# Kernel tuning notes

Measured on AMD Instinct MI355X. Metric: run time of the kernel, lower is better.

The kernel has to match this reference:

```python
import jax, jax.numpy as jnp
import numpy as np

B, T, DIM, DIM_EPS, H = 4, 1024, 2048, 2048, 16
HD = DIM // H        # 128, value head dim
HDE = DIM_EPS // H   # 128, q/k head dim


def setup_inputs() -> dict:
    key = jax.random.key(0)
    ks = jax.random.split(key, 6)
    s = 0.02
    # rotary frequencies as in llama-style precompute (theta=10000)
    inv_freq = 1.0 / (10000.0 ** (np.arange(0, HDE, 2, dtype=np.float32) / HDE))
    t = np.arange(T, dtype=np.float32)
    ang = np.outer(t, inv_freq)  # (T, HDE//2)
    return {
        "v": jax.random.normal(ks[0], (B, T, DIM), jnp.float32),
        "x_eps": jax.random.normal(ks[1], (B, T, DIM_EPS), jnp.float32),
        "freqs_cos": jnp.asarray(np.cos(ang)),
        "freqs_sin": jnp.asarray(np.sin(ang)),
        "W_eps_attn": jax.random.normal(ks[2], (DIM_EPS, 2 * DIM_EPS), jnp.float32) * s,
        "W_attn": jax.random.normal(ks[3], (DIM, DIM), jnp.float32) * s,
        "W_proj": jax.random.normal(ks[4], (DIM, DIM), jnp.float32) * s,
        "W_eps_proj": jax.random.normal(ks[5], (DIM_EPS, DIM_EPS), jnp.float32) * s,
    }


def _rope(x, cos, sin):
    # x: (B, T, H, HDE) -> complex-multiply by freqs_cis of shape (T, HDE//2)
    xr = x.reshape(*x.shape[:-1], -1, 2)
    x_re, x_im = xr[..., 0], xr[..., 1]
    c = cos[None, :, None, :]  # (1, T, 1, HDE//2)
    s = sin[None, :, None, :]
    o_re = x_re * c - x_im * s
    o_im = x_re * s + x_im * c
    return jnp.stack([o_re, o_im], axis=-1).reshape(x.shape)


def reference(v, x_eps, freqs_cos, freqs_sin, W_eps_attn, W_attn, W_proj, W_eps_proj):
    Bn, Tn, C = v.shape
    qk = x_eps @ W_eps_attn            # (B, T, 2*DIM_EPS)
    q, k = jnp.split(qk, 2, axis=-1)
    vp = v @ W_attn                    # (B, T, DIM)
    q = _rope(q.reshape(Bn, Tn, H, HDE), freqs_cos, freqs_sin)
    k = _rope(k.reshape(Bn, Tn, H, HDE), freqs_cos, freqs_sin)
    q = q.transpose(0, 2, 1, 3)        # (B, H, T, HDE)
    k = k.transpose(0, 2, 1, 3)
    vh = vp.reshape(Bn, Tn, H, HD).transpose(0, 2, 1, 3)
    scale = 1.0 / jnp.sqrt(jnp.asarray(HDE, q.dtype))
    scores = jnp.einsum("bhqd,bhkd->bhqk", q, k) * scale
    causal = jnp.tril(jnp.ones((Tn, Tn), bool))
    scores = jnp.where(causal[None, None], scores, jnp.finfo(scores.dtype).min)
    att = jax.nn.softmax(scores, axis=-1)
    y = jnp.einsum("bhqk,bhkd->bhqd", att, vh)
    y = y.transpose(0, 2, 1, 3).reshape(Bn, Tn, C)
    v_out = y @ W_proj
    x_eps_out = x_eps @ W_eps_proj
    return (v_out, x_eps_out)
```

## Files before the change

### kernel.cpp

```cpp
#include <hip/hip_runtime.h>
#include <stdint.h>

typedef __attribute__((ext_vector_type(8))) short  short8;
typedef __attribute__((ext_vector_type(4))) float  f32x4;
typedef __attribute__((ext_vector_type(4))) float  float4v;
typedef __attribute__((ext_vector_type(4))) unsigned short ushort4v;

#define DEV __device__ __forceinline__

DEV unsigned short f2bf(float f) {
    union { float f; unsigned int u; } x; x.f = f;
    unsigned int u = x.u;
    unsigned int r = (u + 0x7fffu + ((u >> 16) & 1u)) >> 16;
    return (unsigned short)r;
}
DEV float bf2f(unsigned short b) {
    union { unsigned int u; float f; } x; x.u = ((unsigned int)b) << 16;
    return x.f;
}

DEV void gll16(const void* g, void* l) {
    __builtin_amdgcn_global_load_lds(
        (const __attribute__((address_space(1))) void*)g,
        (__attribute__((address_space(3))) void*)l, 16, 0, 0);
}

#define MROWS 4096
#define KDIM  2048
#define NQK   4096

__global__ void cast_f32_bf16(const float* __restrict__ in,
                              unsigned short* __restrict__ out, int n4) {
    int i = blockIdx.x * blockDim.x + threadIdx.x;
    if (i < n4) {
        float4v f = ((const float4v*)in)[i];
        ushort4v o;
        o[0] = f2bf(f[0]); o[1] = f2bf(f[1]); o[2] = f2bf(f[2]); o[3] = f2bf(f[3]);
        ((ushort4v*)out)[i] = o;
    }
}

__global__ void transpose_cast(const float* __restrict__ W,
                               unsigned short* __restrict__ Wt, int K, int N) {
    __shared__ float tile[32][33];
    int tx = threadIdx.x, ty = threadIdx.y;
    int n0 = blockIdx.x * 32, k0 = blockIdx.y * 32;
#pragma unroll
    for (int j = 0; j < 32; j += 8)
        tile[ty + j][tx] = W[(size_t)(k0 + ty + j) * N + n0 + tx];
    __syncthreads();
#pragma unroll
    for (int j = 0; j < 32; j += 8)
        Wt[(size_t)(n0 + ty + j) * K + k0 + tx] = f2bf(tile[tx][ty + j]);
}

__global__ void transpose_v(const unsigned short* __restrict__ vp,
                            unsigned short* __restrict__ vpT) {
    __shared__ unsigned short tile[32][34];
    int tx = threadIdx.x, ty = threadIdx.y;
    int R0 = blockIdx.y * 32;
    int c0 = blockIdx.x * 32;
    int bh = R0 >> 7, d0 = R0 & 127;
    int b = bh >> 4, h = bh & 15;
#pragma unroll
    for (int j = 0; j < 32; j += 8)
        tile[ty + j][tx] = vp[(size_t)(b * 1024 + c0 + ty + j) * 2048 + h * 128 + d0 + tx];
    __syncthreads();
#pragma unroll
    for (int j = 0; j < 32; j += 8)
        vpT[(size_t)(R0 + ty + j) * 1024 + c0 + tx] = tile[tx][ty + j];
}

__global__ __launch_bounds__(512, 2) void gemm256(
    const unsigned short* __restrict__ A0g, const unsigned short* __restrict__ B0g,
    float* __restrict__ Cf0, unsigned short* __restrict__ Ch0,
    int N0, int tx0, int nb0, int outbf0,
    const unsigned short* __restrict__ A1g, const unsigned short* __restrict__ B1g,
    float* __restrict__ Cf1, unsigned short* __restrict__ Ch1,
    int N1, int tx1, int outbf1, int K) {

    __shared__ __align__(16) char lds[131072];

    int blk = blockIdx.x;
    const unsigned short* Ag; const unsigned short* Bg;
    float* Cf; unsigned short* Ch; int N, tx, outbf, nwg;
    if (blk < nb0) { Ag = A0g; Bg = B0g; Cf = Cf0; Ch = Ch0; N = N0; tx = tx0; outbf = outbf0; nwg = nb0; }
    else { blk -= nb0; Ag = A1g; Bg = B1g; Cf = Cf1; Ch = Ch1; N = N1; tx = tx1; outbf = outbf1; nwg = gridDim.x - nb0; }
    { int cpx = nwg >> 3; blk = (blk & 7) * cpx + (blk >> 3); }
    const int bx = blk % tx, by = blk / tx;

    const int tid = threadIdx.x;
    const int lane = tid & 63;
    const int w  = tid >> 6;
    const int lr = lane & 15, lk = lane >> 4;
    const int wm = w >> 2, wn = w & 3;
    const int cswz16 = (lk ^ ((lr >> 3) << 1)) * 16;

    const unsigned short* Arow = Ag + (size_t)(by * 256) * K;
    const unsigned short* Brow = Bg + (size_t)(bx * 256) * K;

    auto STAGE = [&](const unsigned short* srcHalf, int k0, char* ldsHalf) {
        int row  = tid >> 2;
        int clog = (tid & 3) ^ (((tid >> 5) & 1) << 1);
        const unsigned short* g = srcHalf + (size_t)row * K + k0 + clog * 8;
        gll16(g,      ldsHalf + tid * 16);
        gll16(g + 32, ldsHalf + 8192 + tid * 16);
    };

    f32x4 acc[8][4];
#pragma unroll
    for (int m = 0; m < 8; ++m)
#pragma unroll
        for (int n = 0; n < 4; ++n) acc[m][n] = (f32x4){0.f, 0.f, 0.f, 0.f};

    const int NT = K >> 6;
    char* buf0 = lds;
    char* buf1 = lds + 65536;

    STAGE(Brow,                   0, buf0 + 32768);
    STAGE(Brow + (size_t)128 * K, 0, buf0 + 32768 + 16384);
    STAGE(Arow,                   0, buf0);
    STAGE(Arow + (size_t)128 * K, 0, buf0 + 16384);
    STAGE(Brow,                  64, buf1 + 32768);
    STAGE(Brow + (size_t)128 * K, 64, buf1 + 32768 + 16384);
    asm volatile("s_waitcnt vmcnt(4)" ::: "memory");
    __builtin_amdgcn_s_barrier();

#define MFMA_BF(a, b, c) __builtin_amdgcn_mfma_f32_16x16x32_bf16(a, b, c, 0, 0, 0)

#define LDAFR(DST, P)                                                                \
    DST[0] = *(const short8*)(aBase +        ((P) * 32 +      lr) * 64 + cswz16);    \
    DST[1] = *(const short8*)(aBase + 8192 + ((P) * 32 +      lr) * 64 + cswz16);    \
    DST[2] = *(const short8*)(aBase +        ((P) * 32 + 16 + lr) * 64 + cswz16);    \
    DST[3] = *(const short8*)(aBase + 8192 + ((P) * 32 + 16 + lr) * 64 + cswz16);

#define MFMA16(P, R)                                                       \
    __builtin_amdgcn_s_setprio(1);                                         \
    _Pragma("unroll")                                                      \
    for (int nf = 0; nf < 4; ++nf) {                                       \
        acc[2*(P)][nf]   = MFMA_BF(R[0], BC[nf][0], acc[2*(P)][nf]);       \
        acc[2*(P)+1][nf] = MFMA_BF(R[2], BC[nf][0], acc[2*(P)+1][nf]);     \
    }                                                                      \
    _Pragma("unroll")                                                      \
    for (int nf = 0; nf < 4; ++nf) {                                       \
        acc[2*(P)][nf]   = MFMA_BF(R[1], BC[nf][1], acc[2*(P)][nf]);       \
        acc[2*(P)+1][nf] = MFMA_BF(R[3], BC[nf][1], acc[2*(P)+1][nf]);     \
    }                                                                      \
    __builtin_amdgcn_s_setprio(0);

    for (int u = 0; u < NT; ++u) {
        char* bufC = (u & 1) ? buf1 : buf0;
        char* bufN = (u & 1) ? buf0 : buf1;
        const char* aBase = bufC + wm * 16384;
        const char* bBase = bufC + 32768 + (wn >> 1) * 16384;
        const int bRow0 = (wn & 1) * 64;
        const bool stA = (u + 1 < NT), stB = (u + 2 < NT);

        short8 BC[4][2];
#pragma unroll
        for (int nf = 0; nf < 4; ++nf) {
            BC[nf][0] = *(const short8*)(bBase +        (bRow0 + nf * 16 + lr) * 64 + cswz16);
            BC[nf][1] = *(const short8*)(bBase + 8192 + (bRow0 + nf * 16 + lr) * 64 + cswz16);
        }
        short8 Ra[4], Rb[4];
        LDAFR(Ra, 0)
        LDAFR(Rb, 1)
        if (stA) STAGE(Arow, (u + 1) * 64, bufN);
        asm volatile("s_waitcnt lgkmcnt(4)" ::: "memory");
        __builtin_amdgcn_s_barrier();
        MFMA16(0, Ra)
        __builtin_amdgcn_s_barrier();

        LDAFR(Ra, 2)
        if (stA) STAGE(Arow + (size_t)128 * K, (u + 1) * 64, bufN + 16384);
        asm volatile("s_waitcnt lgkmcnt(4)" ::: "memory");
        __builtin_amdgcn_s_barrier();
        MFMA16(1, Rb)
        __builtin_amdgcn_s_barrier();

        LDAFR(Rb, 3)
        if (stB) STAGE(Brow, (u + 2) * 64, bufC + 32768);
        asm volatile("s_waitcnt lgkmcnt(4)" ::: "memory");
        __builtin_amdgcn_s_barrier();
        MFMA16(2, Ra)
        __builtin_amdgcn_s_barrier();

        if (stB) STAGE(Brow + (size_t)128 * K, (u + 2) * 64, bufC + 32768 + 16384);
        asm volatile("s_waitcnt lgkmcnt(0)" ::: "memory");
        __builtin_amdgcn_s_barrier();
        MFMA16(3, Rb)
        if (stB) { asm volatile("s_waitcnt vmcnt(4)" ::: "memory"); }
        else     { asm volatile("s_waitcnt vmcnt(0)" ::: "memory"); }
        __builtin_amdgcn_s_barrier();
    }
#undef LDAFR
#undef MFMA16

    if (outbf) {
#pragma unroll
        for (int mf = 0; mf < 8; ++mf)
#pragma unroll
            for (int nf = 0; nf < 4; ++nf)
#pragma unroll
                for (int r = 0; r < 4; ++r) {
                    int row = by * 256 + wm * 128 + mf * 16 + lk * 4 + r;
                    int col = bx * 256 + wn * 64 + nf * 16 + lr;
                    Ch[(size_t)row * N + col] = f2bf(acc[mf][nf][r]);
                }
    } else {
#pragma unroll
        for (int mf = 0; mf < 8; ++mf)
#pragma unroll
            for (int nf = 0; nf < 4; ++nf)
#pragma unroll
                for (int r = 0; r < 4; ++r) {
                    int row = by * 256 + wm * 128 + mf * 16 + lk * 4 + r;
                    int col = bx * 256 + wn * 64 + nf * 16 + lr;
                    Cf[(size_t)row * N + col] = acc[mf][nf][r];
                }
    }
}

__global__ void rope_kernel(unsigned short* __restrict__ qk,
                            const float* __restrict__ fcos,
                            const float* __restrict__ fsin) {
    int idx  = blockIdx.x * 256 + threadIdx.x;
    int row  = idx >> 9;
    int g    = idx & 511;
    int t    = row & 1023;
    int half = g >> 8;
    int hp   = g & 255;
    int h    = hp >> 4;
    int ig   = hp & 15;
    int col  = half * 2048 + h * 128 + ig * 8;
    size_t off = (size_t)row * 4096 + col;

    short8 v = *(short8*)(qk + off);
    int i0 = ig * 4;
    float4v c = *(const float4v*)(fcos + t * 64 + i0);
    float4v s = *(const float4v*)(fsin + t * 64 + i0);
    short8 o;
#pragma unroll
    for (int p = 0; p < 4; ++p) {
        float re = bf2f((unsigned short)v[2 * p]);
        float im = bf2f((unsigned short)v[2 * p + 1]);
        o[2 * p]     = (short)f2bf(re * c[p] - im * s[p]);
        o[2 * p + 1] = (short)f2bf(re * s[p] + im * c[p]);
    }
    *(short8*)(qk + off) = o;
}

__global__ __launch_bounds__(256) void attn_kernel(
    const unsigned short* __restrict__ qk,
    const unsigned short* __restrict__ vpT,
    unsigned short* __restrict__ y) {

    const int bh = blockIdx.x;
    const int qt = 7 - (int)blockIdx.y;
    const int b = bh >> 4, h = bh & 15;
    const int qb0 = qt * 128;

    __shared__ __align__(16) unsigned short Kt[64 * 128];
    __shared__ __align__(16) unsigned short Vt[128 * 64];
    __shared__ __align__(16) unsigned short Pl[4 * 32 * 72];

    const int tid = threadIdx.x, w = tid >> 6, lane = tid & 63;
    const int lr = lane & 15, lk = lane >> 4;

    const unsigned short* Qb = qk + (size_t)(b * 1024) * 4096 + h * 128;
    const unsigned short* Kb = Qb + 2048;
    const unsigned short* Vg = vpT + (size_t)bh * 128 * 1024;
    unsigned short* Pw = &Pl[w * 32 * 72];

    short8 qf[2][4];
#pragma unroll
    for (int m = 0; m < 2; ++m) {
        const unsigned short* qrow = Qb + (size_t)(qb0 + w * 32 + m * 16 + lr) * 4096;
#pragma unroll
        for (int db = 0; db < 4; ++db)
            qf[m][db] = *(const short8*)(qrow + db * 32 + lk * 8);
    }

    f32x4 acc[2][8];
#pragma unroll
    for (int m = 0; m < 2; ++m)
#pragma unroll
        for (int n = 0; n < 8; ++n) acc[m][n] = (f32x4){0.f, 0.f, 0.f, 0.f};
    float m_i[2][4], l_i[2][4];
#pragma unroll
    for (int m = 0; m < 2; ++m)
#pragma unroll
        for (int r = 0; r < 4; ++r) { m_i[m][r] = -1e30f; l_i[m][r] = 0.f; }

    const int nkt = 2 * qt + 2;
    for (int kt = 0; kt < nkt; ++kt) {
#pragma unroll
        for (int c = 0; c < 4; ++c) {
            int base = w * 4096 + c * 1024;
            int row  = (base >> 8) + (lane >> 4);
            int colB = (lane & 15) * 16;
            int scol = colB ^ ((row & 7) << 4);
            gll16(Kb + (size_t)(kt * 64 + row) * 4096 + (scol >> 1),
                  (char*)Kt + base);
        }
#pragma unroll
        for (int c = 0; c < 4; ++c) {
            int base = w * 4096 + c * 1024;
            int d    = (base >> 7) + (lane >> 3);
            int colB = (lane & 7) * 16;
            int scol = colB ^ ((d & 7) << 4);
            gll16(Vg + (size_t)d * 1024 + kt * 64 + (scol >> 1),
                  (char*)Vt + base);
        }
        __syncthreads();

        f32x4 s[2][4];
#pragma unroll
        for (int m = 0; m < 2; ++m)
#pragma unroll
            for (int n = 0; n < 4; ++n) s[m][n] = (f32x4){0.f, 0.f, 0.f, 0.f};
#pragma unroll
        for (int db = 0; db < 4; ++db)
#pragma unroll
            for (int n = 0; n < 4; ++n) {
                int krow = n * 16 + lr;
                int cb = (db * 64 + lk * 16) ^ ((krow & 7) << 4);
                short8 kf = *(const short8*)((const char*)Kt + krow * 256 + cb);
                s[0][n] = __builtin_amdgcn_mfma_f32_16x16x32_bf16(qf[0][db], kf, s[0][n], 0, 0, 0);
                s[1][n] = __builtin_amdgcn_mfma_f32_16x16x32_bf16(qf[1][db], kf, s[1][n], 0, 0, 0);
            }

        const float sc = 0.08838834764831845f;
        const bool diag = (kt >= 2 * qt);
#pragma unroll
        for (int m = 0; m < 2; ++m)
#pragma unroll
            for (int n = 0; n < 4; ++n)
#pragma unroll
                for (int r = 0; r < 4; ++r) {
                    float v = s[m][n][r] * sc;
                    if (diag) {
                        int q   = qb0 + w * 32 + m * 16 + lk * 4 + r;
                        int key = kt * 64 + n * 16 + lr;
                        if (key > q) v = -1e30f;
                    }
                    s[m][n][r] = v;
                }

#pragma unroll
        for (int m = 0; m < 2; ++m) {
            float pm[4];
#pragma unroll
            for (int r = 0; r < 4; ++r)
                pm[r] = fmaxf(fmaxf(s[m][0][r], s[m][1][r]), fmaxf(s[m][2][r], s[m][3][r]));
#pragma unroll
            for (int o = 1; o < 16; o <<= 1)
#pragma unroll
                for (int r = 0; r < 4; ++r)
                    pm[r] = fmaxf(pm[r], __shfl_xor(pm[r], o, 16));

            float resc[4], rs[4];
#pragma unroll
            for (int r = 0; r < 4; ++r) {
                float mn = fmaxf(m_i[m][r], pm[r]);
                resc[r] = __expf(m_i[m][r] - mn);
                m_i[m][r] = mn;
                rs[r] = 0.f;
            }
#pragma unroll
            for (int n = 0; n < 4; ++n)
#pragma unroll
                for (int r = 0; r < 4; ++r) {
                    float p = __expf(s[m][n][r] - m_i[m][r]);
                    s[m][n][r] = p;
                    rs[r] += p;
                }
#pragma unroll
            for (int o = 1; o < 16; o <<= 1)
#pragma unroll
                for (int r = 0; r < 4; ++r)
                    rs[r] += __shfl_xor(rs[r], o, 16);
#pragma unroll
            for (int r = 0; r < 4; ++r)
                l_i[m][r] = l_i[m][r] * resc[r] + rs[r];
#pragma unroll
            for (int n = 0; n < 8; ++n)
#pragma unroll
                for (int r = 0; r < 4; ++r)
                    acc[m][n][r] *= resc[r];

#pragma unroll
            for (int n = 0; n < 4; ++n)
#pragma unroll
                for (int r = 0; r < 4; ++r)
                    Pw[(m * 16 + lk * 4 + r) * 72 + n * 16 + lr] = f2bf(s[m][n][r]);
        }

#pragma unroll
        for (int ks = 0; ks < 2; ++ks) {
            short8 pf0 = *(const short8*)&Pw[(lr) * 72 + ks * 32 + lk * 8];
            short8 pf1 = *(const short8*)&Pw[(16 + lr) * 72 + ks * 32 + lk * 8];
#pragma unroll
            for (int n8 = 0; n8 < 8; ++n8) {
                int d  = n8 * 16 + lr;
                int cb = (ks * 64 + lk * 16) ^ ((d & 7) << 4);
                short8 vf = *(const short8*)((const char*)Vt + d * 128 + cb);
                acc[0][n8] = __builtin_amdgcn_mfma_f32_16x16x32_bf16(pf0, vf, acc[0][n8], 0, 0, 0);
                acc[1][n8] = __builtin_amdgcn_mfma_f32_16x16x32_bf16(pf1, vf, acc[1][n8], 0, 0, 0);
            }
        }
        __syncthreads();
    }

    unsigned short* yb = y + (size_t)(b * 1024) * 2048 + h * 128;
#pragma unroll
    for (int m = 0; m < 2; ++m)
#pragma unroll
        for (int n8 = 0; n8 < 8; ++n8)
#pragma unroll
            for (int r = 0; r < 4; ++r) {
                int t = qb0 + w * 32 + m * 16 + lk * 4 + r;
                int d = n8 * 16 + lr;
                yb[(size_t)t * 2048 + d] = f2bf(acc[m][n8][r] / l_i[m][r]);
            }
}

extern "C" void kernel_launch(void* const* d_in, const int* in_sizes, int n_in,
                              void* d_out, int out_size, void* d_ws, size_t ws_size,
                              hipStream_t stream) {
    const float* v_in  = (const float*)d_in[0];
    const float* xeps  = (const float*)d_in[1];
    const float* fcos  = (const float*)d_in[2];
    const float* fsin  = (const float*)d_in[3];
    const float* Wea   = (const float*)d_in[4];
    const float* Wa    = (const float*)d_in[5];
    const float* Wp    = (const float*)d_in[6];
    const float* Wep   = (const float*)d_in[7];
    float* out = (float*)d_out;

    char* ws = (char*)d_ws;
    unsigned short* xe16 = (unsigned short*)ws;  ws += (size_t)MROWS * KDIM * 2;
    unsigned short* v16  = (unsigned short*)ws;  ws += (size_t)MROWS * KDIM * 2;
    unsigned short* WeaT = (unsigned short*)ws;  ws += (size_t)NQK * KDIM * 2;
    unsigned short* WaT  = (unsigned short*)ws;  ws += (size_t)KDIM * KDIM * 2;
    unsigned short* WpT  = (unsigned short*)ws;  ws += (size_t)KDIM * KDIM * 2;
    unsigned short* WepT = (unsigned short*)ws;  ws += (size_t)KDIM * KDIM * 2;
    unsigned short* qk16 = (unsigned short*)ws;  ws += (size_t)MROWS * NQK * 2;
    unsigned short* vp16 = (unsigned short*)ws;  ws += (size_t)MROWS * KDIM * 2;
    unsigned short* y16  = (unsigned short*)ws;  ws += (size_t)MROWS * KDIM * 2;
    unsigned short* vpT  = v16;

    cast_f32_bf16<<<8192, 256, 0, stream>>>(xeps, xe16, MROWS * KDIM / 4);
    cast_f32_bf16<<<8192, 256, 0, stream>>>(v_in, v16,  MROWS * KDIM / 4);

    transpose_cast<<<dim3(NQK / 32, KDIM / 32), dim3(32, 8), 0, stream>>>(Wea, WeaT, KDIM, NQK);
    transpose_cast<<<dim3(KDIM / 32, KDIM / 32), dim3(32, 8), 0, stream>>>(Wa,  WaT,  KDIM, KDIM);
    transpose_cast<<<dim3(KDIM / 32, KDIM / 32), dim3(32, 8), 0, stream>>>(Wp,  WpT,  KDIM, KDIM);
    transpose_cast<<<dim3(KDIM / 32, KDIM / 32), dim3(32, 8), 0, stream>>>(Wep, WepT, KDIM, KDIM);

    gemm256<<<256, 512, 0, stream>>>(
        xe16, WeaT, nullptr, qk16, NQK, 16, 256, 1,
        xe16, WeaT, nullptr, qk16, NQK, 16, 1, KDIM);

    rope_kernel<<<8192, 256, 0, stream>>>(qk16, fcos, fsin);

    gemm256<<<256, 512, 0, stream>>>(
        v16,  WaT,  nullptr, vp16, KDIM, 8, 128, 1,
        xe16, WepT, out + (size_t)MROWS * KDIM, nullptr, KDIM, 8, 0, KDIM);

    transpose_v<<<dim3(1024 / 32, 8192 / 32), dim3(32, 8), 0, stream>>>(vp16, vpT);

    attn_kernel<<<dim3(64, 8), 256, 0, stream>>>(qk16, vpT, y16);

    gemm256<<<128, 512, 0, stream>>>(
        y16, WpT, out, nullptr, KDIM, 8, 128, 0,
        y16, WpT, out, nullptr, KDIM, 8, 0, KDIM);
}
```

Baseline: 330.9 us.

## Restructure GEMM main loop into register double-buffered LDS reads with cross-iteration prefetch

Rewrites the bf16 GEMM inner loop so A and B fragments are read from LDS in 4-fragment groups into ping-pong register sets, and the first fragments of the next k-tile are prefetched during the last phase of the current one. Global-to-LDS staging is reshuffled across phases with precomputed pointers and clamped k offsets instead of conditional staging, plus sched_barrier fences. The intent is to hide LDS read latency behind MFMAs and cut address arithmetic. In exchange it holds more fragments in registers, does redundant loads at the tail, and has more delicate waitcnt/barrier ordering.

```diff
diff --git a/kernel.cpp b/kernel.cpp
--- a/kernel.cpp
+++ b/kernel.cpp
@@ -95,17 +95,27 @@
     const int lr = lane & 15, lk = lane >> 4;
     const int wm = w >> 2, wn = w & 3;
     const int cswz16 = (lk ^ ((lr >> 3) << 1)) * 16;
+    const int rdOff  = lr * 64 + cswz16;
+    const int bRow0B = (wn & 1) * 4096;
 
     const unsigned short* Arow = Ag + (size_t)(by * 256) * K;
     const unsigned short* Brow = Bg + (size_t)(bx * 256) * K;
 
-    auto STAGE = [&](const unsigned short* srcHalf, int k0, char* ldsHalf) {
-        int row  = tid >> 2;
-        int clog = (tid & 3) ^ (((tid >> 5) & 1) << 1);
-        const unsigned short* g = srcHalf + (size_t)row * K + k0 + clog * 8;
-        gll16(g,      ldsHalf + tid * 16);
-        gll16(g + 32, ldsHalf + 8192 + tid * 16);
-    };
+    const int srow = tid >> 2;
+    const int sclog = (tid & 3) ^ (((tid >> 5) & 1) << 1);
+    const unsigned short* aSt0 = Arow + (size_t)srow * K + sclog * 8;
+    const unsigned short* aSt1 = aSt0 + (size_t)128 * K;
+    const unsigned short* bSt0 = Brow + (size_t)srow * K + sclog * 8;
+    const unsigned short* bSt1 = bSt0 + (size_t)128 * K;
+
+    char* sA0 = lds;            char* sB0 = lds + 32768;
+    char* sA1 = lds + 65536;    char* sB1 = lds + 98304;
+    const int sOff = tid * 16;
+
+    const char* aB0 = lds + wm * 16384;
+    const char* aB1 = aB0 + 65536;
+    const char* bB0 = lds + 32768 + (wn >> 1) * 16384;
+    const char* bB1 = bB0 + 65536;
 
     f32x4 acc[8][4];
 #pragma unroll
@@ -114,87 +124,97 @@
         for (int n = 0; n < 4; ++n) acc[m][n] = (f32x4){0.f, 0.f, 0.f, 0.f};
 
     const int NT = K >> 6;
-    char* buf0 = lds;
-    char* buf1 = lds + 65536;
-
-    STAGE(Brow,                   0, buf0 + 32768);
-    STAGE(Brow + (size_t)128 * K, 0, buf0 + 32768 + 16384);
-    STAGE(Arow,                   0, buf0);
-    STAGE(Arow + (size_t)128 * K, 0, buf0 + 16384);
-    STAGE(Brow,                  64, buf1 + 32768);
-    STAGE(Brow + (size_t)128 * K, 64, buf1 + 32768 + 16384);
-    asm volatile("s_waitcnt vmcnt(4)" ::: "memory");
+
+    gll16(bSt0,      sB0 + sOff);                 gll16(bSt0 + 32, sB0 + 8192 + sOff);
+    gll16(bSt1,      sB0 + 16384 + sOff);         gll16(bSt1 + 32, sB0 + 16384 + 8192 + sOff);
+    gll16(aSt0,      sA0 + sOff);                 gll16(aSt0 + 32, sA0 + 8192 + sOff);
+    gll16(aSt1,      sA0 + 16384 + sOff);         gll16(aSt1 + 32, sA0 + 16384 + 8192 + sOff);
+    gll16(bSt0 + 64, sB1 + sOff);                 gll16(bSt0 + 96, sB1 + 8192 + sOff);
+    asm volatile("s_waitcnt vmcnt(2)" ::: "memory");
     __builtin_amdgcn_s_barrier();
 
 #define MFMA_BF(a, b, c) __builtin_amdgcn_mfma_f32_16x16x32_bf16(a, b, c, 0, 0, 0)
 
-#define LDAFR(DST, P)                                                                \
-    DST[0] = *(const short8*)(aBase +        ((P) * 32 +      lr) * 64 + cswz16);    \
-    DST[1] = *(const short8*)(aBase + 8192 + ((P) * 32 +      lr) * 64 + cswz16);    \
-    DST[2] = *(const short8*)(aBase +        ((P) * 32 + 16 + lr) * 64 + cswz16);    \
-    DST[3] = *(const short8*)(aBase + 8192 + ((P) * 32 + 16 + lr) * 64 + cswz16);
-
-#define MFMA16(P, R)                                                       \
-    __builtin_amdgcn_s_setprio(1);                                         \
-    _Pragma("unroll")                                                      \
-    for (int nf = 0; nf < 4; ++nf) {                                       \
-        acc[2*(P)][nf]   = MFMA_BF(R[0], BC[nf][0], acc[2*(P)][nf]);       \
-        acc[2*(P)+1][nf] = MFMA_BF(R[2], BC[nf][0], acc[2*(P)+1][nf]);     \
-    }                                                                      \
-    _Pragma("unroll")                                                      \
-    for (int nf = 0; nf < 4; ++nf) {                                       \
-        acc[2*(P)][nf]   = MFMA_BF(R[1], BC[nf][1], acc[2*(P)][nf]);       \
-        acc[2*(P)+1][nf] = MFMA_BF(R[3], BC[nf][1], acc[2*(P)+1][nf]);     \
-    }                                                                      \
+#define LD4A(DST, BASE, KS, MH)                                                  \
+    DST[0] = *(const short8*)((BASE) + (KS) * 8192 + (MH) * 4096 +    0 + rdOff); \
+    DST[1] = *(const short8*)((BASE) + (KS) * 8192 + (MH) * 4096 + 1024 + rdOff); \
+    DST[2] = *(const short8*)((BASE) + (KS) * 8192 + (MH) * 4096 + 2048 + rdOff); \
+    DST[3] = *(const short8*)((BASE) + (KS) * 8192 + (MH) * 4096 + 3072 + rdOff);
+
+#define LD4B(DST, BASE, KS)                                                               \
+    DST[0] = *(const short8*)((BASE) + (KS) * 8192 + bRow0B +    0 + rdOff);              \
+    DST[1] = *(const short8*)((BASE) + (KS) * 8192 + bRow0B + 1024 + rdOff);              \
+    DST[2] = *(const short8*)((BASE) + (KS) * 8192 + bRow0B + 2048 + rdOff);              \
+    DST[3] = *(const short8*)((BASE) + (KS) * 8192 + bRow0B + 3072 + rdOff);
+
+#define MFMA16(MH, AR, BR)                                                  \
+    __builtin_amdgcn_s_setprio(1);                                          \
+    _Pragma("unroll")                                                       \
+    for (int i = 0; i < 4; ++i)                                             \
+        _Pragma("unroll")                                                   \
+        for (int nf = 0; nf < 4; ++nf)                                      \
+            acc[(MH) * 4 + i][nf] = MFMA_BF(AR[i], BR[nf], acc[(MH) * 4 + i][nf]); \
     __builtin_amdgcn_s_setprio(0);
 
+#define PHASE_SYNC                                          \
+    asm volatile("s_waitcnt lgkmcnt(8)" ::: "memory");      \
+    __builtin_amdgcn_s_barrier();                           \
+    __builtin_amdgcn_sched_barrier(0);
+
+    short8 Ax[4], Ay[4], Bx[4], By[4];
+    LD4A(Ax, aB0, 0, 0)
+    LD4B(Bx, bB0, 0)
+
     for (int u = 0; u < NT; ++u) {
-        char* bufC = (u & 1) ? buf1 : buf0;
-        char* bufN = (u & 1) ? buf0 : buf1;
-        const char* aBase = bufC + wm * 16384;
-        const char* bBase = bufC + 32768 + (wn >> 1) * 16384;
-        const int bRow0 = (wn & 1) * 64;
-        const bool stA = (u + 1 < NT), stB = (u + 2 < NT);
-
-        short8 BC[4][2];
-#pragma unroll
-        for (int nf = 0; nf < 4; ++nf) {
-            BC[nf][0] = *(const short8*)(bBase +        (bRow0 + nf * 16 + lr) * 64 + cswz16);
-            BC[nf][1] = *(const short8*)(bBase + 8192 + (bRow0 + nf * 16 + lr) * 64 + cswz16);
-        }
-        short8 Ra[4], Rb[4];
-        LDAFR(Ra, 0)
-        LDAFR(Rb, 1)
-        if (stA) STAGE(Arow, (u + 1) * 64, bufN);
-        asm volatile("s_waitcnt lgkmcnt(4)" ::: "memory");
+        const bool par = u & 1;
+        const char* aC = par ? aB1 : aB0;
+        const char* bC = par ? bB1 : bB0;
+        const char* aN = par ? aB0 : aB1;
+        const char* bN = par ? bB0 : bB1;
+        char* dAN = par ? sA0 : sA1;
+        char* dBN = par ? sB0 : sB1;
+        char* dBC = par ? sB1 : sB0;
+        const int kA  = (u + 1 < NT ? u + 1 : NT - 1) * 64;
+        const int kB2 = (u + 2 < NT ? u + 2 : NT - 1) * 64;
+
+        LD4A(Ay, aC, 1, 0)
+        LD4B(By, bC, 1)
+        gll16(bSt1 + kA,      dBN + 16384 + sOff);
+        gll16(bSt1 + kA + 32, dBN + 16384 + 8192 + sOff);
+        gll16(aSt0 + kA,      dAN + sOff);
+        gll16(aSt0 + kA + 32, dAN + 8192 + sOff);
+        gll16(aSt1 + kA,      dAN + 16384 + sOff);
+        gll16(aSt1 + kA + 32, dAN + 16384 + 8192 + sOff);
+        PHASE_SYNC
+        MFMA16(0, Ax, Bx)
         __builtin_amdgcn_s_barrier();
-        MFMA16(0, Ra)
+
+        LD4A(Ax, aC, 0, 1)
+        LD4B(Bx, bC, 0)
+        PHASE_SYNC
+        MFMA16(0, Ay, By)
         __builtin_amdgcn_s_barrier();
 
-        LDAFR(Ra, 2)
-        if (stA) STAGE(Arow + (size_t)128 * K, (u + 1) * 64, bufN + 16384);
-        asm volatile("s_waitcnt lgkmcnt(4)" ::: "memory");
+        LD4A(Ay, aC, 1, 1)
+        LD4B(By, bC, 1)
+        PHASE_SYNC
+        MFMA16(1, Ax, Bx)
+        asm volatile("s_waitcnt vmcnt(0)" ::: "memory");
         __builtin_amdgcn_s_barrier();
-        MFMA16(1, Rb)
+
+        LD4A(Ax, aN, 0, 0)
+        LD4B(Bx, bN, 0)
+        gll16(bSt0 + kB2,      dBC + sOff);
+        gll16(bSt0 + kB2 + 32, dBC + 8192 + sOff);
+        PHASE_SYNC
+        MFMA16(1, Ay, By)
         __builtin_amdgcn_s_barrier();
-
-        LDAFR(Rb, 3)
-        if (stB) STAGE(Brow, (u + 2) * 64, bufC + 32768);
-        asm volatile("s_waitcnt lgkmcnt(4)" ::: "memory");
-        __builtin_amdgcn_s_barrier();
-        MFMA16(2, Ra)
-        __builtin_amdgcn_s_barrier();
-
-        if (stB) STAGE(Brow + (size_t)128 * K, (u + 2) * 64, bufC + 32768 + 16384);
-        asm volatile("s_waitcnt lgkmcnt(0)" ::: "memory");
-        __builtin_amdgcn_s_barrier();
-        MFMA16(3, Rb)
-        if (stB) { asm volatile("s_waitcnt vmcnt(4)" ::: "memory"); }
-        else     { asm volatile("s_waitcnt vmcnt(0)" ::: "memory"); }
-        __builtin_amdgcn_s_barrier();
-    }
-#undef LDAFR
+    }
+    asm volatile("s_waitcnt vmcnt(0)" ::: "memory");
+#undef LD4A
+#undef LD4B
 #undef MFMA16
+#undef PHASE_SYNC
 
     if (outbf) {
 #pragma unroll
```

Measured after the change: 338.2 us. 2.2% more time.
